# Kernel tuning notes

Hardware: AMD Instinct MI355X
Metric: run time of the kernel (lower is better)

## Reference

```python
import jax, jax.numpy as jnp
import numpy as np

N_CLUSTERS = 2048
MAX_ITER = 5


def setup_inputs() -> dict:
    key = jax.random.key(0)
    k1, k2 = jax.random.split(key)
    X = jax.random.normal(k1, (131072, 128), dtype=jnp.float32)
    init_centroids = jax.random.normal(k2, (N_CLUSTERS, 128), dtype=jnp.float32)
    return {"X": X, "init_centroids": init_centroids}


def _euc_sim(a, b):
    # 2 a.b^T - |a|^2 - |b|^2  (negative squared euclidean distance)
    return (2.0 * (a @ b.T)
            - jnp.sum(a * a, axis=1)[:, None]
            - jnp.sum(b * b, axis=1)[None, :])


def reference(X, init_centroids):
    K = init_centroids.shape[0]

    def step(centroids, _):
        sim = _euc_sim(X, centroids)              # [N, K]
        closest = jnp.argmax(sim, axis=-1)         # [N]
        sums = jax.ops.segment_sum(X, closest, num_segments=K)        # [K, d]
        counts = jax.ops.segment_sum(jnp.ones_like(closest, dtype=X.dtype),
                                     closest, num_segments=K)         # [K]
        # full-batch branch: c_grad = mask @ x / mask.sum(-1), NaN -> 0
        c_grad = jnp.where(counts[:, None] > 0, sums / jnp.maximum(counts, 1.0)[:, None], 0.0)
        # minibatch is None => lr = 1 => centroids <- c_grad
        return c_grad, closest

    centroids, closest_hist = jax.lax.scan(step, init_centroids, None, length=MAX_ITER)
    labels = closest_hist[-1]
    return centroids, labels
```

## Files before the change

kernel.cpp:

```cpp
#include <hip/hip_runtime.h>
#include <hip/hip_bf16.h>

#define NP 131072
#define D 128
#define KC 2048
#define ITERS 5
#define CG 8

#define TAU 0.015f
#define CNOFF 49152

#if defined(__has_builtin)
#if __has_builtin(__builtin_amdgcn_global_load_lds)
#define USE_GLL 1
#endif
#endif

typedef short bf16x8 __attribute__((ext_vector_type(8)));
typedef float f32x4 __attribute__((ext_vector_type(4)));

__device__ inline unsigned short f2bf(float x) {
    __hip_bfloat16 b = __float2bfloat16(x);
    return *reinterpret_cast<unsigned short*>(&b);
}
__device__ inline float bf2f(unsigned short u) {
    union { unsigned int i; float f; } c; c.i = ((unsigned int)u) << 16; return c.f;
}

__device__ inline size_t pslot(int k, int d, int hl) {
    int g = k >> 4, t15 = k & 15, ks = d >> 5, q = (d >> 3) & 3, e = d & 7;
    return ((size_t)((ks * 128 + g) * 2 + hl)) * 512 + (q * 16 + t15) * 8 + e;
}

#if USE_GLL
#define GLL16(srcp, dstp) __builtin_amdgcn_global_load_lds( \
    (const __attribute__((address_space(1))) unsigned int*)(srcp), \
    (__attribute__((address_space(3))) unsigned int*)(dstp), 16, 0, 0)
#define GLL4(srcp, dstp) __builtin_amdgcn_global_load_lds( \
    (const __attribute__((address_space(1))) unsigned int*)(srcp), \
    (__attribute__((address_space(3))) unsigned int*)(dstp), 4, 0, 0)
#else
#define GLL16(srcp, dstp) do { *(uint4*)((char*)(dstp) + lane * 16) = *(const uint4*)(srcp); } while (0)
#define GLL4(srcp, dstp)  do { *(unsigned int*)((char*)(dstp) + lane * 4) = *(const unsigned int*)(srcp); } while (0)
#endif

__global__ void init_kernel(const float* __restrict__ initC,
                            double* __restrict__ C64, double* __restrict__ CT64,
                            unsigned short* __restrict__ Pn,
                            double* __restrict__ cn64, float* __restrict__ cn32,
                            int* __restrict__ counter) {
    __shared__ double sred[4];
    int tid = threadIdx.x;
    int t = blockIdx.x * 256 + tid;
    float v = initC[t];
    double dv = (double)v;
    C64[t] = dv;
    CT64[(size_t)(t & 127) * KC + (t >> 7)] = dv;
    unsigned short h = f2bf(v);
    int k = t >> 7, d = t & 127;
    Pn[pslot(k, d, 0)] = h;
    Pn[pslot(k, d, 1)] = f2bf(v - bf2f(h));
    double s = dv * dv;
#pragma unroll
    for (int m = 1; m < 64; m <<= 1) s += __shfl_xor(s, m, 64);
    if ((tid & 63) == 0) sred[tid >> 6] = s;
    __syncthreads();
    if (tid == 0)   { double ss = sred[0] + sred[1]; cn64[k] = ss; cn32[k] = (float)ss; }
    if (tid == 128) { double ss = sred[2] + sred[3]; cn64[k] = ss; cn32[k] = (float)ss; }
    if (blockIdx.x == 0 && tid == 0) *counter = 0;
}

__global__ __launch_bounds__(256, 3)
void assign_kernel(const float* __restrict__ X,
                   const unsigned short* __restrict__ Pn,
                   const float* __restrict__ cnorm,
                   int* __restrict__ labels,
                   int* __restrict__ list,
                   int* __restrict__ counter) {
    __shared__ __align__(16) char lds[49664];

    const int tid = threadIdx.x;
    const int lane = tid & 63;
    const int wid = tid >> 6;
    const int wrow = wid >> 1;
    const int wcol = wid & 1;
    const int t15 = lane & 15;
    const int q = lane >> 4;
    const int pbase = blockIdx.x * 64;
    const char* PnB = (const char*)Pn;

#pragma unroll
    for (int i = 0; i < 8; i++) {
        int f = i * 256 + tid;
        int row = f >> 5, c4 = f & 31;
        float4 v = *(const float4*)&X[(size_t)(pbase + row) * D + c4 * 4];
        unsigned short h0 = f2bf(v.x), h1 = f2bf(v.y), h2 = f2bf(v.z), h3 = f2bf(v.w);
        unsigned short l0 = f2bf(v.x - bf2f(h0)), l1 = f2bf(v.y - bf2f(h1));
        unsigned short l2 = f2bf(v.z - bf2f(h2)), l3 = f2bf(v.w - bf2f(h3));
        uint2 ph = { (unsigned)h0 | ((unsigned)h1 << 16), (unsigned)h2 | ((unsigned)h3 << 16) };
        uint2 pl = { (unsigned)l0 | ((unsigned)l1 << 16), (unsigned)l2 | ((unsigned)l3 << 16) };
        int ad = (row * 256 + c4 * 8) ^ ((row & 7) << 4);
        *(uint2*)(lds + ad) = ph;
        *(uint2*)(lds + 16384 + ad) = pl;
    }
    __syncthreads();

    bf16x8 rah[2][4], ral[2][4];
#pragma unroll
    for (int rt = 0; rt < 2; rt++) {
        int row = wrow * 32 + rt * 16 + t15;
        int sw = (row & 7) << 4;
#pragma unroll
        for (int ks = 0; ks < 4; ks++) {
            int ad = (row * 256 + ks * 64 + q * 16) ^ sw;
            rah[rt][ks] = *(const bf16x8*)(lds + ad);
            ral[rt][ks] = *(const bf16x8*)(lds + 16384 + ad);
        }
    }
    __syncthreads();

    float b1[8], b2[8];
    int i1[8];
#pragma unroll
    for (int s = 0; s < 8; s++) { b1[s] = -INFINITY; b2[s] = -INFINITY; i1[s] = 0x7fffffff; }

#pragma unroll
    for (int i = 0; i < 4; i++) {
        int seg = wid * 4 + i;
        GLL16(PnB + seg * 1024 + lane * 16, lds + seg * 1024);
    }
#pragma unroll
    for (int i = 0; i < 4; i++) {
        int seg = wid * 4 + i;
        GLL16(PnB + (size_t)(1 * 128) * 2048 + seg * 1024 + lane * 16,
              lds + 16384 + seg * 1024);
    }

#define STEP(KS, VMSTR) do {                                                  \
        asm volatile("s_waitcnt vmcnt(" VMSTR ")" ::: "memory");              \
        __builtin_amdgcn_s_barrier();                                         \
        asm volatile("" ::: "memory");                                        \
        __builtin_amdgcn_sched_barrier(0);                                    \
        int t_ = ct * 4 + (KS);                                               \
        int s2_ = t_ + 2;                                                     \
        int s2c_ = (s2_ > 63) ? 63 : s2_;                                     \
        char* bstage_ = lds + (unsigned)(s2_ % 3) * 16384;                    \
        const char* nsrc_ = PnB + ((size_t)((s2c_ & 3) * 128 + (s2c_ >> 2) * 8)) * 2048; \
        _Pragma("unroll")                                                     \
        for (int i_ = 0; i_ < 4; i_++) {                                      \
            int seg_ = wid * 4 + i_;                                          \
            GLL16(nsrc_ + seg_ * 1024 + lane * 16, bstage_ + seg_ * 1024);    \
        }                                                                     \
        if ((KS) == 0) {                                                      \
            const float* cs_ = cnorm + ct * 128;                              \
            GLL4(cs_ + lane, lds + CNOFF);                                    \
            GLL4(cs_ + 64 + lane, lds + CNOFF + 256);                         \
        }                                                                     \
        const char* bcur_ = lds + (unsigned)(t_ % 3) * 16384;                 \
        __builtin_amdgcn_s_setprio(1);                                        \
        _Pragma("unroll")                                                     \
        for (int cj_ = 0; cj_ < 4; cj_++) {                                   \
            int gl_ = wcol * 4 + cj_;                                         \
            bf16x8 bh_ = *(const bf16x8*)(bcur_ + gl_ * 2048 + lane * 16);    \
            bf16x8 bl_ = *(const bf16x8*)(bcur_ + gl_ * 2048 + 1024 + lane * 16); \
            _Pragma("unroll")                                                 \
            for (int rt_ = 0; rt_ < 2; rt_++) {                               \
                acc[rt_][cj_] = __builtin_amdgcn_mfma_f32_16x16x32_bf16(rah[rt_][KS], bh_, acc[rt_][cj_], 0, 0, 0); \
                acc[rt_][cj_] = __builtin_amdgcn_mfma_f32_16x16x32_bf16(rah[rt_][KS], bl_, acc[rt_][cj_], 0, 0, 0); \
                acc[rt_][cj_] = __builtin_amdgcn_mfma_f32_16x16x32_bf16(ral[rt_][KS], bh_, acc[rt_][cj_], 0, 0, 0); \
            }                                                                 \
        }                                                                     \
        __builtin_amdgcn_s_setprio(0);                                        \
    } while (0)

    for (int ct = 0; ct < KC / 128; ct++) {
        f32x4 acc[2][4];
#pragma unroll
        for (int rt = 0; rt < 2; rt++)
#pragma unroll
            for (int cj = 0; cj < 4; cj++) acc[rt][cj] = (f32x4){0.f, 0.f, 0.f, 0.f};

        STEP(0, "4");
        STEP(1, "6");
        STEP(2, "6");
        STEP(3, "4");

        const float* cnL = (const float*)(lds + CNOFF);
#pragma unroll
        for (int cj = 0; cj < 4; cj++) {
            int col = ct * 128 + wcol * 64 + cj * 16 + t15;
            float cnv = cnL[wcol * 64 + cj * 16 + t15];
#pragma unroll
            for (int rt = 0; rt < 2; rt++)
#pragma unroll
                for (int rg = 0; rg < 4; rg++) {
                    int s = rt * 4 + rg;
                    float sv = __builtin_fmaf(2.0f, acc[rt][cj][rg], -cnv);
                    bool gt1 = sv > b1[s];
                    float mx2 = fmaxf(b2[s], sv);
                    b2[s] = gt1 ? b1[s] : mx2;
                    i1[s] = gt1 ? col : i1[s];
                    b1[s] = gt1 ? sv : b1[s];
                }
        }
    }
#undef STEP

#pragma unroll
    for (int s = 0; s < 8; s++) {
#pragma unroll
        for (int m = 1; m < 16; m <<= 1) {
            float ob1 = __shfl_xor(b1[s], m, 64);
            int   oi  = __shfl_xor(i1[s], m, 64);
            float ob2 = __shfl_xor(b2[s], m, 64);
            bool gt = ob1 > b1[s];
            bool eq = ob1 == b1[s];
            float nb2 = gt ? fmaxf(b1[s], ob2) : fmaxf(b2[s], ob1);
            nb2 = eq ? b1[s] : nb2;
            int ni = gt ? oi : i1[s];
            ni = (eq && oi < i1[s]) ? oi : ni;
            b1[s] = gt ? ob1 : b1[s];
            b2[s] = nb2;
            i1[s] = ni;
        }
    }

    __syncthreads();
    float* mb1 = (float*)lds;
    float* mb2 = ((float*)lds) + 128;
    int*   mi1 = (int*)(((float*)lds) + 256);
    if (t15 == 0) {
#pragma unroll
        for (int rt = 0; rt < 2; rt++)
#pragma unroll
            for (int rg = 0; rg < 4; rg++) {
                int s = rt * 4 + rg;
                int row = wrow * 32 + rt * 16 + q * 4 + rg;
                mb1[wcol * 64 + row] = b1[s];
                mb2[wcol * 64 + row] = b2[s];
                mi1[wcol * 64 + row] = i1[s];
            }
    }
    __syncthreads();
    if (tid < 64) {
        float a1 = mb1[tid], a2 = mb2[tid];  int ai = mi1[tid];
        float c1 = mb1[64 + tid], c2 = mb2[64 + tid];  int ci = mi1[64 + tid];
        float best, second;  int bi;
        if (a1 > c1)      { best = a1; bi = ai; second = fmaxf(a2, c1); }
        else if (a1 < c1) { best = c1; bi = ci; second = fmaxf(c2, a1); }
        else              { best = a1; bi = (ai < ci) ? ai : ci; second = a1; }
        int p = pbase + tid;
        labels[p] = bi;
        if (best - second < TAU) {
            int idx = atomicAdd(counter, 1);
            list[idx] = p;
        }
    }
}

__global__ void recheck_kernel(const float* __restrict__ X,
                               const double* __restrict__ CT64,
                               const double* __restrict__ cn64,
                               const int* __restrict__ list,
                               const int* __restrict__ counter,
                               int* __restrict__ labels) {
    __shared__ float xrow[D];
    __shared__ double rb[4];
    __shared__ int ri[4];
    int cnt = *counter;
    for (int ii = blockIdx.x; ii < cnt; ii += gridDim.x) {
        int p = list[ii];
        __syncthreads();
        if (threadIdx.x < D) xrow[threadIdx.x] = X[(size_t)p * D + threadIdx.x];
        __syncthreads();
        double xn = 0.0;
#pragma unroll 16
        for (int d = 0; d < D; d++) {
            double xv = (double)xrow[d];
            xn = fma(xv, xv, xn);
        }
        double best = -1.0e300;
        int bi = 0x7fffffff;
#pragma unroll
        for (int g = 0; g < 8; g++) {
            int c = threadIdx.x + 256 * g;
            double acc = 0.0;
#pragma unroll 16
            for (int d = 0; d < D; d++)
                acc = fma((double)xrow[d], CT64[(size_t)d * KC + c], acc);
            double s = 2.0 * acc - xn - cn64[c];
            if (s > best || (s == best && c < bi)) { best = s; bi = c; }
        }
#pragma unroll
        for (int m = 1; m < 64; m <<= 1) {
            double ob = __shfl_xor(best, m, 64);
            int oi = __shfl_xor(bi, m, 64);
            if (ob > best || (ob == best && oi < bi)) { best = ob; bi = oi; }
        }
        int w = threadIdx.x >> 6;
        if ((threadIdx.x & 63) == 0) { rb[w] = best; ri[w] = bi; }
        __syncthreads();
        if (threadIdx.x == 0) {
            double bb = rb[0]; int bbi = ri[0];
            for (int w2 = 1; w2 < 4; w2++)
                if (rb[w2] > bb || (rb[w2] == bb && ri[w2] < bbi)) { bb = rb[w2]; bbi = ri[w2]; }
            labels[p] = bbi;
        }
    }
}

__global__ __launch_bounds__(512)
void accum_kernel(const float* __restrict__ X,
                  const int* __restrict__ labels,
                  double* __restrict__ C64, double* __restrict__ CT64,
                  unsigned short* __restrict__ Pn,
                  double* __restrict__ cn64, float* __restrict__ cn32,
                  int* __restrict__ counter,
                  float* __restrict__ outC) {
    __shared__ double sred[8][CG][64][2];
    __shared__ int cred[8][CG];
    __shared__ int cntS[CG];
    __shared__ double cnp[2][8];
    const int lane = threadIdx.x & 63;
    const int w = threadIdx.x >> 6;
    const int kbase = blockIdx.x * CG;
    const int base0 = w * (NP / 8);
    double s0[CG], s1[CG];
    int cnt[CG];
#pragma unroll
    for (int c = 0; c < CG; c++) { s0[c] = 0.0; s1[c] = 0.0; cnt[c] = 0; }

    for (int it = 0; it < (NP / 8) / 256; it++) {
        int4 lab = *(const int4*)&labels[base0 + it * 256 + lane * 4];
#pragma unroll
        for (int j = 0; j < 4; j++) {
            int lv = (j == 0) ? lab.x : (j == 1) ? lab.y : (j == 2) ? lab.z : lab.w;
            int rel = lv - kbase;
#pragma unroll
            for (int c = 0; c < CG; c++) {
                unsigned long long m = __ballot(rel == c);
                cnt[c] += __popcll(m);
                while (m) {
                    int b = __ffsll(m) - 1;
                    m &= m - 1;
                    int p = base0 + it * 256 + b * 4 + j;
                    float2 v = *(const float2*)&X[(size_t)p * D + lane * 2];
                    s0[c] += (double)v.x;
                    s1[c] += (double)v.y;
                }
            }
        }
    }
#pragma unroll
    for (int c = 0; c < CG; c++) {
        sred[w][c][lane][0] = s0[c];
        sred[w][c][lane][1] = s1[c];
    }
    if (lane < CG) cred[w][lane] = cnt[lane];
    __syncthreads();

    if (threadIdx.x < CG) {
        int s = 0;
#pragma unroll
        for (int ww = 0; ww < 8; ww++) s += cred[ww][threadIdx.x];
        cntS[threadIdx.x] = s;
    }
    __syncthreads();

#pragma unroll
    for (int rep = 0; rep < 2; rep++) {
        int idx = rep * 512 + threadIdx.x;
        int c = idx >> 7, d = idx & 127;
        double s = 0.0;
#pragma unroll
        for (int ww = 0; ww < 8; ww++) s += sred[ww][c][d >> 1][d & 1];
        int k = kbase + c;
        int n = cntS[c];
        double v = (n > 0) ? s / (double)n : 0.0;
        C64[(size_t)k * D + d] = v;
        CT64[(size_t)d * KC + k] = v;
        float vf = (float)v;
        unsigned short h = f2bf(vf);
        Pn[pslot(k, d, 0)] = h;
        Pn[pslot(k, d, 1)] = f2bf(vf - bf2f(h));
        if (outC) outC[(size_t)k * D + d] = vf;
        double sq = v * v;
#pragma unroll
        for (int m = 1; m < 64; m <<= 1) sq += __shfl_xor(sq, m, 64);
        if (lane == 0) cnp[rep][w] = sq;
    }
    __syncthreads();
    if (threadIdx.x < CG) {
        int c = threadIdx.x;
        int rep = c >> 2, wp = (c & 3) * 2;
        double cn = cnp[rep][wp] + cnp[rep][wp + 1];
        cn64[kbase + c] = cn;
        cn32[kbase + c] = (float)cn;
    }
    if (blockIdx.x == 0 && threadIdx.x == 0) *counter = 0;
}

__global__ void lab2f_kernel(const int* __restrict__ labels, float* __restrict__ out) {
    int t = blockIdx.x * 256 + threadIdx.x;
    out[t] = (float)labels[t];
}

extern "C" void kernel_launch(void* const* d_in, const int* in_sizes, int n_in,
                              void* d_out, int out_size, void* d_ws, size_t ws_size,
                              hipStream_t stream) {
    const float* X = (const float*)d_in[0];
    const float* initC = (const float*)d_in[1];
    float* out = (float*)d_out;

    char* w = (char*)d_ws;
    const size_t MB = 1u << 20;
    double* C64    = (double*)(w);
    double* CT64   = (double*)(w + 4 * MB);
    unsigned short* Pn = (unsigned short*)(w + 6 * MB);
    int*    labels = (int*)   (w + 7 * MB);
    int*    list   = (int*)   (w + 7 * MB + 512 * 1024);
    double* cn64   = (double*)(w + 8 * MB);
    float*  cn32   = (float*) (w + 8 * MB + 16 * 1024);
    int*    counter= (int*)   (w + 8 * MB + 32 * 1024);

    init_kernel<<<(KC * D) / 256, 256, 0, stream>>>(initC, C64, CT64, Pn, cn64, cn32, counter);

    for (int it = 0; it < ITERS; it++) {
        assign_kernel<<<NP / 64, 256, 0, stream>>>(X, Pn, cn32, labels, list, counter);
        recheck_kernel<<<2048, 256, 0, stream>>>(X, CT64, cn64, list, counter, labels);
        accum_kernel<<<KC / CG, 512, 0, stream>>>(X, labels, C64, CT64, Pn, cn64, cn32,
                                                  counter, (it == ITERS - 1) ? out : nullptr);
    }
    lab2f_kernel<<<NP / 256, 256, 0, stream>>>(labels, out + (size_t)KC * D);
}
```

Baseline: 1.845 ms.

## Batch four points per block in fp64 recheck and use med3 for top-2 tracking

The fp64 recheck kernel now handles four candidate points per block iteration. Each CT64 centroid load is reused across four accumulators, which cuts global traffic per point, and the point norms are computed with a wave reduction. The main distance kernel's top-2 update is simplified with fmed3 and fmax, removing some selects. Register pressure in the recheck rises, and tie handling in the top-2 path changes slightly, since the second-best value now comes from a median.

```diff
diff --git a/kernel.cpp b/kernel.cpp
--- a/kernel.cpp
+++ b/kernel.cpp
@@ -196,11 +196,11 @@
                 for (int rg = 0; rg < 4; rg++) {
                     int s = rt * 4 + rg;
                     float sv = __builtin_fmaf(2.0f, acc[rt][cj][rg], -cnv);
+                    float nb2 = __builtin_amdgcn_fmed3f(b1[s], b2[s], sv);
                     bool gt1 = sv > b1[s];
-                    float mx2 = fmaxf(b2[s], sv);
-                    b2[s] = gt1 ? b1[s] : mx2;
                     i1[s] = gt1 ? col : i1[s];
-                    b1[s] = gt1 ? sv : b1[s];
+                    b1[s] = fmaxf(b1[s], sv);
+                    b2[s] = nb2;
                 }
         }
     }
@@ -258,53 +258,88 @@
     }
 }
 
-__global__ void recheck_kernel(const float* __restrict__ X,
-                               const double* __restrict__ CT64,
-                               const double* __restrict__ cn64,
-                               const int* __restrict__ list,
-                               const int* __restrict__ counter,
-                               int* __restrict__ labels) {
-    __shared__ float xrow[D];
-    __shared__ double rb[4];
-    __shared__ int ri[4];
+__global__ __launch_bounds__(256)
+void recheck_kernel(const float* __restrict__ X,
+                    const double* __restrict__ CT64,
+                    const double* __restrict__ cn64,
+                    const int* __restrict__ list,
+                    const int* __restrict__ counter,
+                    int* __restrict__ labels) {
+    __shared__ float xrow[4][D];
+    __shared__ double xnS[4];
+    __shared__ double rb[4][4];
+    __shared__ int ri[4][4];
+    const int tid = threadIdx.x;
+    const int lane = tid & 63;
+    const int w = tid >> 6;
     int cnt = *counter;
-    for (int ii = blockIdx.x; ii < cnt; ii += gridDim.x) {
-        int p = list[ii];
+    for (int base = blockIdx.x * 4; base < cnt; base += gridDim.x * 4) {
+        int np4 = (cnt - base < 4) ? (cnt - base) : 4;
         __syncthreads();
-        if (threadIdx.x < D) xrow[threadIdx.x] = X[(size_t)p * D + threadIdx.x];
+#pragma unroll
+        for (int j = 0; j < 2; j++) {
+            int idx = j * 256 + tid;
+            int r = idx >> 7, d = idx & 127;
+            if (r < np4) xrow[r][d] = X[(size_t)list[base + r] * D + d];
+        }
         __syncthreads();
-        double xn = 0.0;
-#pragma unroll 16
-        for (int d = 0; d < D; d++) {
-            double xv = (double)xrow[d];
-            xn = fma(xv, xv, xn);
-        }
-        double best = -1.0e300;
-        int bi = 0x7fffffff;
+        {
+            double xx = 0.0;
+            if (w < np4) {
+                float2 v = *(const float2*)&xrow[w][lane * 2];
+                xx = (double)v.x * (double)v.x + (double)v.y * (double)v.y;
+            }
+#pragma unroll
+            for (int m = 1; m < 64; m <<= 1) xx += __shfl_xor(xx, m, 64);
+            if (lane == 0) xnS[w] = xx;
+        }
+        __syncthreads();
+
+        double best[4]; int bi[4];
+#pragma unroll
+        for (int p = 0; p < 4; p++) { best[p] = -1.0e300; bi[p] = 0x7fffffff; }
+
 #pragma unroll
         for (int g = 0; g < 8; g++) {
-            int c = threadIdx.x + 256 * g;
-            double acc = 0.0;
-#pragma unroll 16
-            for (int d = 0; d < D; d++)
-                acc = fma((double)xrow[d], CT64[(size_t)d * KC + c], acc);
-            double s = 2.0 * acc - xn - cn64[c];
-            if (s > best || (s == best && c < bi)) { best = s; bi = c; }
-        }
-#pragma unroll
-        for (int m = 1; m < 64; m <<= 1) {
-            double ob = __shfl_xor(best, m, 64);
-            int oi = __shfl_xor(bi, m, 64);
-            if (ob > best || (ob == best && oi < bi)) { best = ob; bi = oi; }
-        }
-        int w = threadIdx.x >> 6;
-        if ((threadIdx.x & 63) == 0) { rb[w] = best; ri[w] = bi; }
+            int c = tid + 256 * g;
+            double acc[4];
+#pragma unroll
+            for (int p = 0; p < 4; p++) acc[p] = 0.0;
+#pragma unroll 4
+            for (int d = 0; d < D; d++) {
+                double wv = CT64[(size_t)d * KC + c];
+#pragma unroll
+                for (int p = 0; p < 4; p++)
+                    acc[p] = fma((double)xrow[p][d], wv, acc[p]);
+            }
+            double cn = cn64[c];
+#pragma unroll
+            for (int p = 0; p < 4; p++) {
+                double s = 2.0 * acc[p] - xnS[p] - cn;
+                if (s > best[p] || (s == best[p] && c < bi[p])) { best[p] = s; bi[p] = c; }
+            }
+        }
+
+#pragma unroll
+        for (int p = 0; p < 4; p++)
+#pragma unroll
+            for (int m = 1; m < 64; m <<= 1) {
+                double ob = __shfl_xor(best[p], m, 64);
+                int oi = __shfl_xor(bi[p], m, 64);
+                if (ob > best[p] || (ob == best[p] && oi < bi[p])) { best[p] = ob; bi[p] = oi; }
+            }
+        if (lane == 0) {
+#pragma unroll
+            for (int p = 0; p < 4; p++) { rb[w][p] = best[p]; ri[w][p] = bi[p]; }
+        }
         __syncthreads();
-        if (threadIdx.x == 0) {
-            double bb = rb[0]; int bbi = ri[0];
+        if (tid < np4) {
+            int p = tid;
+            double bb = rb[0][p]; int bbi = ri[0][p];
+#pragma unroll
             for (int w2 = 1; w2 < 4; w2++)
-                if (rb[w2] > bb || (rb[w2] == bb && ri[w2] < bbi)) { bb = rb[w2]; bbi = ri[w2]; }
-            labels[p] = bbi;
+                if (rb[w2][p] > bb || (rb[w2][p] == bb && ri[w2][p] < bbi)) { bb = rb[w2][p]; bbi = ri[w2][p]; }
+            labels[list[base + p]] = bbi;
         }
     }
 }
```

Measured after the change: 2.350 ms. 27.4% more time.
